# Kernel tuning notes

Hardware: AMD Instinct MI355X
Metric: run time of the kernel (lower is better)

The kernel has to match this reference:

```python
import math
import jax, jax.numpy as jnp
import numpy as np

RMS_EPS = 1.1920929e-07  # torch.finfo(float32).eps used by F.rms_norm default

def _rms_norm(x):
    return x * jax.lax.rsqrt(jnp.mean(jnp.square(x), axis=-1, keepdims=True) + RMS_EPS)

def _rope(x, cos, sin):
    # x: [B,T,H,D]; cos/sin: [T, D//2]
    d = x.shape[-1] // 2
    x1, x2 = x[..., :d], x[..., d:]
    c = cos[None, :, None, :]
    s = sin[None, :, None, :]
    return jnp.concatenate([x1 * c + x2 * s, -x1 * s + x2 * c], axis=-1).astype(x.dtype)

def setup_inputs():
    key = jax.random.key(0)
    ks = jax.random.split(key, 8)
    B, T, C, H, D = 2, 2048, 2048, 16, 128
    x = jax.random.normal(ks[0], (B, T, C), dtype=jnp.float32)
    # real RoPE tables for [T, D//2]
    half = D // 2
    inv_freq = 1.0 / (10000.0 ** (np.arange(half, dtype=np.float32) / half))
    ang = np.outer(np.arange(T, dtype=np.float32), inv_freq)
    cos = jnp.asarray(np.cos(ang), dtype=jnp.float32)
    sin = jnp.asarray(np.sin(ang), dtype=jnp.float32)
    s = 0.02
    Wq = jax.random.normal(ks[1], (C, H * D), dtype=jnp.float32) * s
    Wk = jax.random.normal(ks[2], (C, H * D), dtype=jnp.float32) * s
    Wv = jax.random.normal(ks[3], (C, H * D), dtype=jnp.float32) * s
    Wo = jax.random.normal(ks[4], (C, C), dtype=jnp.float32) * s
    fgate_w = jax.random.normal(ks[5], (C, H), dtype=jnp.float32) * s
    fgate_b = jnp.zeros((H,), dtype=jnp.float32)
    weight_lambda = jax.random.normal(ks[6], (C, H), dtype=jnp.float32) * s
    return dict(x=x, cos=cos, sin=sin, Wq=Wq, Wk=Wk, Wv=Wv, Wo=Wo,
                fgate_w=fgate_w, fgate_b=fgate_b, weight_lambda=weight_lambda,
                window_size=1024)

def reference(x, cos, sin, Wq, Wk, Wv, Wo, fgate_w, fgate_b, weight_lambda, window_size):
    B, T, C = x.shape
    H = fgate_w.shape[1]
    D = Wq.shape[1] // H
    sm_scale = 1.0 / math.sqrt(D)
    # QKV projections (bias=False)
    q = (x @ Wq).reshape(B, T, H, D)
    k = (x @ Wk).reshape(B, T, H, D)
    v = (x @ Wv).reshape(B, T, H, D)
    # RoPE then parameter-free RMSNorm on q,k
    q = _rms_norm(_rope(q, cos, sin))
    k = _rms_norm(_rope(k, cos, sin))
    # [B,H,T,D]
    q = q.transpose(0, 2, 1, 3)
    k = k.transpose(0, 2, 1, 3)
    v = v.transpose(0, 2, 1, 3)
    # forgetting gate: log f_t per (B,H,T)
    lam = jax.nn.elu((x @ weight_lambda).astype(jnp.float32)) + 1.0          # [B,T,H]
    logit = (x @ fgate_w + fgate_b) * lam                                    # [B,T,H]
    log_fgate = (jax.nn.log_sigmoid(logit) / (lam + 0.001)).transpose(0, 2, 1)  # [B,H,T]
    cumF = jnp.cumsum(log_fgate, axis=-1)                                    # [B,H,T]
    # forgetting flash attention, dense reference: bias_ij = cumF_i - cumF_j
    scores = jnp.einsum('bhqd,bhkd->bhqk', q.astype(jnp.float32), k.astype(jnp.float32)) * sm_scale
    scores = scores + cumF[..., :, None] - cumF[..., None, :]
    i = jnp.arange(T)[:, None]
    j = jnp.arange(T)[None, :]
    allowed = (j <= i) & (i - j < window_size)  # causal + sliding window
    scores = jnp.where(allowed, scores, -jnp.inf)
    attn = jax.nn.softmax(scores, axis=-1)
    y = jnp.einsum('bhqk,bhkd->bhqd', attn, v.astype(jnp.float32)).astype(x.dtype)
    y = y.transpose(0, 2, 1, 3).reshape(B, T, C)
    return y @ Wo
```

## Files before the change

### kernel.cpp

```cpp
#include <hip/hip_runtime.h>
#include <hip/hip_bf16.h>
#include <stdint.h>

#define T_SEQ 2048
#define CDIM  2048
#define NHEAD 16
#define DHEAD 128
#define BT    4096
#define BHT   32
#define NQKV  6144

typedef __bf16 bf16x8_t __attribute__((ext_vector_type(8)));
typedef float  f32x4_t  __attribute__((ext_vector_type(4)));
typedef unsigned short u16x8_t __attribute__((ext_vector_type(8)));
typedef unsigned short u16x4_t __attribute__((ext_vector_type(4)));

__device__ __forceinline__ unsigned short f2bf(float f){
  unsigned int u = __float_as_uint(f);
  u += 0x7fffu + ((u >> 16) & 1u);
  return (unsigned short)(u >> 16);
}
__device__ __forceinline__ float bf2f(unsigned short h){
  return __uint_as_float(((unsigned int)h) << 16);
}
__device__ __forceinline__ unsigned ldsaddr(const void* p){
  return (unsigned)(size_t)(const __attribute__((address_space(3))) void*)p;
}
__device__ __forceinline__ u16x4_t tr16(unsigned a){
  u16x4_t r;
  asm volatile("ds_read_b64_tr_b16 %0, %1" : "=v"(r) : "v"(a));
  return r;
}

__global__ __launch_bounds__(256) void transpose_cast(const float* __restrict__ W,
                                                      unsigned short* __restrict__ Wt){
  __shared__ float tile[32][33];
  int n0 = blockIdx.x*32, k0 = blockIdx.y*32;
  int tx = threadIdx.x, ty = threadIdx.y;
  #pragma unroll
  for (int i=0;i<32;i+=8)
    tile[ty+i][tx] = W[(size_t)(k0+ty+i)*CDIM + n0 + tx];
  __syncthreads();
  #pragma unroll
  for (int i=0;i<32;i+=8)
    Wt[(size_t)(n0+ty+i)*CDIM + k0 + tx] = f2bf(tile[tx][ty+i]);
}

__global__ __launch_bounds__(256) void build_wgt(const float* __restrict__ fgw,
                                                 const float* __restrict__ wlam,
                                                 float* __restrict__ WgT){
  int idx = blockIdx.x*256 + threadIdx.x;
  int c = idx >> 11, k = idx & 2047;
  const float* W = (c < 16) ? fgw : wlam;
  WgT[idx] = W[k*16 + (c & 15)];
}


#define V3_SYNC() do{ __builtin_amdgcn_sched_barrier(0); \
  __builtin_amdgcn_s_barrier(); \
  asm volatile("s_waitcnt lgkmcnt(0)" ::: "memory"); \
  __builtin_amdgcn_sched_barrier(0); }while(0)

#define V3_TAIL() do{ asm volatile("s_waitcnt vmcnt(3)" ::: "memory"); \
  __builtin_amdgcn_sched_barrier(0); \
  __builtin_amdgcn_s_barrier(); }while(0)

#define V3_MFMA() do{ __builtin_amdgcn_s_setprio(1); \
  _Pragma("unroll") for (int mi=0;mi<4;mi++) \
  _Pragma("unroll") for (int ni=0;ni<4;ni++) \
    acc[mi][ni] = __builtin_amdgcn_mfma_f32_16x16x32_bf16(af[mi], bfr[ni], acc[mi][ni],0,0,0); \
  __builtin_amdgcn_s_setprio(0); }while(0)

#define V3_PHASE(BUF, TIDX) do{ \
  readA(BUF); readB(BUF); \
  { int ts_ = (TIDX)+2; if (ts_ > ntm1) ts_ = ntm1; stage(((BUF)+2)%3, ts_); } \
  V3_SYNC(); V3_MFMA(); V3_TAIL(); }while(0)

template<int MODE>
__global__ __launch_bounds__(512, 2) void gemm_v3(const unsigned short* __restrict__ A,
                                                  const unsigned short* __restrict__ Bt,
                                                  void* __restrict__ Cout,
                                                  int M, int N, int K){
  extern __shared__ unsigned short lds[];
  const int nx = N >> 8;
  const int Mt = M >> 7;
  const int bid = blockIdx.x;
  const int c8 = bid & 7, w = bid >> 3;
  const int mh = Mt >> 1;
  const int mt = (c8 & 1)*mh + (w % mh);
  const int ntc = (c8 >> 1)*(nx >> 2) + (w / mh);
  const int m0 = mt << 7, n0 = ntc << 8;
  const int tid = threadIdx.x, lane = tid & 63, wv = tid >> 6;
  const int wm = wv >> 2, wn = wv & 3;
  const int g = lane >> 4, qi = lane & 15;
  const int ntm1 = (K >> 5) - 1;

  f32x4_t acc[4][4] = {};
  bf16x8_t af[4], bfr[4];

  int goffA, goffB[2];
  { int s = tid; int row = s >> 2; int lg = (s & 3) ^ ((row >> 1) & 3);
    goffA = row*K + lg*8; }
  #pragma unroll
  for (int j=0;j<2;j++){
    int s = j*512 + tid;
    int row = s >> 2;
    int lg = (s & 3) ^ ((row >> 1) & 3);
    goffB[j] = row*K + lg*8;
  }

  auto stage = [&](int buf, int kt){
    const unsigned short* srcA = A + (size_t)m0*K + kt*32;
    const unsigned short* srcB = Bt + (size_t)n0*K + kt*32;
    unsigned short* base = lds + buf*12288;
    __builtin_amdgcn_global_load_lds(
        (const __attribute__((address_space(1))) void*)(srcA + goffA),
        (__attribute__((address_space(3))) void*)(base + tid*8), 16, 0, 0);
    #pragma unroll
    for (int j=0;j<2;j++)
      __builtin_amdgcn_global_load_lds(
        (const __attribute__((address_space(1))) void*)(srcB + goffB[j]),
        (__attribute__((address_space(3))) void*)(base + 4096 + (j*512 + tid)*8), 16, 0, 0);
  };
  auto readA = [&](int buf){
    const unsigned short* base = lds + buf*12288;
    #pragma unroll
    for (int mi=0;mi<4;mi++){
      int row = wm*64 + mi*16 + qi;
      int gs = g ^ ((row >> 1) & 3);
      af[mi] = *reinterpret_cast<const bf16x8_t*>(base + (row*4 + gs)*8);
    }
  };
  auto readB = [&](int buf){
    const unsigned short* base = lds + buf*12288 + 4096;
    #pragma unroll
    for (int ni=0;ni<4;ni++){
      int row = wn*64 + ni*16 + qi;
      int gs = g ^ ((row >> 1) & 3);
      bfr[ni] = *reinterpret_cast<const bf16x8_t*>(base + (row*4 + gs)*8);
    }
  };

  stage(0,0); stage(1,1);
  asm volatile("s_waitcnt vmcnt(3)" ::: "memory");
  __builtin_amdgcn_sched_barrier(0);
  __builtin_amdgcn_s_barrier();

  for (int it=0; it<21; ++it){
    const int t3 = it*3;
    V3_PHASE(0, t3+0);
    V3_PHASE(1, t3+1);
    V3_PHASE(2, t3+2);
  }
  V3_PHASE(0, 63);
  asm volatile("s_waitcnt vmcnt(0)" ::: "memory");

  #pragma unroll
  for (int mi=0;mi<4;mi++){
    #pragma unroll
    for (int ni=0;ni<4;ni++){
      #pragma unroll
      for (int r=0;r<4;r++){
        int mm = m0 + wm*64 + mi*16 + 4*g + r;
        int nn = n0 + wn*64 + ni*16 + qi;
        float v = acc[mi][ni][r];
        if (MODE == 2){
          ((float*)Cout)[(size_t)mm*N + nn] = v;
        } else {
          int bb2 = mm >> 11, t = mm & (T_SEQ-1);
          int which = nn >> 11;
          int hh = (nn >> 7) & 15, d = nn & (DHEAD-1);
          ((unsigned short*)Cout)[(size_t)which*8388608 +
              (((size_t)bb2*NHEAD + hh)*T_SEQ + t)*DHEAD + d] = f2bf(v);
        }
      }
    }
  }
}

#define GROWS 4
__global__ __launch_bounds__(256) void gates_kernel(const float* __restrict__ x,
    const float* __restrict__ WgT, const float* __restrict__ fgb,
    float* __restrict__ lfg, unsigned short* __restrict__ xb){
  __shared__ float xs[GROWS*2048];
  __shared__ float part[GROWS*32*8];
  const int r0 = blockIdx.x*GROWS;
  const int tid = threadIdx.x;
  const float* xp = x + (size_t)r0*CDIM;
  #pragma unroll
  for (int i=0;i<GROWS*2048/(256*4); i++){
    int e = (i*256+tid)*4;
    *(float4*)(xs+e) = *(const float4*)(xp+e);
  }
  __syncthreads();
  #pragma unroll
  for (int i=0;i<GROWS*2048/(256*8); i++){
    int e = (i*256+tid)*8;
    u16x8_t ob;
    #pragma unroll
    for (int j=0;j<8;j++) ob[j] = f2bf(xs[e+j]);
    *reinterpret_cast<u16x8_t*>(xb + (size_t)r0*CDIM + e) = ob;
  }
  const int c = tid & 31, kseg = tid >> 5;
  const float* wp = WgT + c*2048 + kseg*256;
  const float* xq = xs + kseg*256;
  f32x4_t acc[GROWS] = {};
  for (int kk=0; kk<64; kk++){
    f32x4_t wv = *(const f32x4_t*)(wp + kk*4);
    #pragma unroll
    for (int r=0;r<GROWS;r++){
      f32x4_t xv = *(const f32x4_t*)(xq + r*2048 + kk*4);
      acc[r] += xv*wv;
    }
  }
  #pragma unroll
  for (int r=0;r<GROWS;r++)
    part[(r*32 + c)*8 + kseg] = acc[r][0]+acc[r][1]+acc[r][2]+acc[r][3];
  __syncthreads();
  if (tid < GROWS*32){
    const int r = tid >> 5, c2 = tid & 31;
    const float* pp = part + (r*32+c2)*8;
    float s = pp[0]+pp[1]+pp[2]+pp[3]+pp[4]+pp[5]+pp[6]+pp[7];
    float other = __shfl_xor(s, 16, 64);
    if (c2 < 16){
      float df = s, dl = other;
      float lam = (dl > 0.f) ? (dl + 1.f) : __expf(dl);
      float logit = (df + fgb[c2]) * lam;
      float ls = fminf(logit, 0.f) - log1pf(__expf(-fabsf(logit)));
      float lf = ls / (lam + 0.001f);
      int row = r0 + r;
      int b = row >> 11, t = row & (T_SEQ-1);
      lfg[((size_t)b*NHEAD + c2)*T_SEQ + t] = lf;
    }
  }
}

__global__ __launch_bounds__(256) void cumsum_kernel(const float* __restrict__ lfg,
                                                     float* __restrict__ cumF){
  __shared__ float sums[256];
  const int bh = blockIdx.x;
  const float* in = lfg + (size_t)bh*T_SEQ;
  float* out = cumF + (size_t)bh*T_SEQ;
  const int tid = threadIdx.x;
  float4 a = *(const float4*)(in + tid*8);
  float4 b = *(const float4*)(in + tid*8 + 4);
  float v[8] = {a.x,a.y,a.z,a.w,b.x,b.y,b.z,b.w};
  float run = 0.f;
  #pragma unroll
  for (int e=0;e<8;e++) run += v[e];
  sums[tid] = run;
  __syncthreads();
  for (int off=1; off<256; off<<=1){
    float y = (tid >= off) ? sums[tid-off] : 0.f;
    __syncthreads();
    sums[tid] += y;
    __syncthreads();
  }
  float acc = sums[tid] - run;
  float o[8];
  #pragma unroll
  for (int e=0;e<8;e++){ acc += v[e]; o[e] = acc; }
  *(float4*)(out + tid*8)     = make_float4(o[0],o[1],o[2],o[3]);
  *(float4*)(out + tid*8 + 4) = make_float4(o[4],o[5],o[6],o[7]);
}

__global__ __launch_bounds__(256) void rope_rms(unsigned short* __restrict__ QK,
    const float* __restrict__ cosT, const float* __restrict__ sinT){
  const int tid = threadIdx.x, lane = tid & 63, wv = tid >> 6;
  const int idx2 = blockIdx.x*4 + wv;
  const int which = idx2 >> 16;
  const int row = idx2 & 65535;
  const int t = row & (T_SEQ-1);
  unsigned short* xp = QK + (size_t)which*8388608 + (size_t)row*DHEAD;
  float x1 = bf2f(xp[lane]);
  float x2 = bf2f(xp[lane+64]);
  float c = cosT[t*64 + lane];
  float s = sinT[t*64 + lane];
  float o1 = x1*c + x2*s;
  float o2 = x2*c - x1*s;
  float ss = o1*o1 + o2*o2;
  #pragma unroll
  for (int off=1; off<64; off<<=1) ss += __shfl_xor(ss, off, 64);
  float scale = rsqrtf(ss*(1.f/128.f) + 1.1920929e-07f);
  xp[lane]    = f2bf(o1*scale);
  xp[lane+64] = f2bf(o2*scale);
}

__global__ __launch_bounds__(256, 2) void attn_kernel(const unsigned short* __restrict__ Qh,
    const unsigned short* __restrict__ Kh, const unsigned short* __restrict__ Vh,
    const float* __restrict__ cumF, unsigned short* __restrict__ Y,
    const int* __restrict__ winp){
  __shared__ unsigned short smem[32768];
  const int dlin = blockIdx.y*16 + blockIdx.x;
  const int c8 = dlin & 7, klin = dlin >> 3;
  const int bh = c8 + 8*(klin >> 4);
  const int q0b = (klin & 15)*128;
  const int b = bh >> 4, h = bh & 15;
  const int tid = threadIdx.x, lane = tid & 63, wv = tid >> 6;
  const int g = lane >> 4, qi = lane & 15;
  const int win = *winp;
  const unsigned short* Qp = Qh + (size_t)bh*T_SEQ*DHEAD;
  const unsigned short* Kp = Kh + (size_t)bh*T_SEQ*DHEAD;
  const unsigned short* Vp = Vh + (size_t)bh*T_SEQ*DHEAD;
  const float* cF = cumF + (size_t)bh*T_SEQ;
  const int q0w = q0b + wv*32;
  bf16x8_t qf[2][4];
  float cFq[2];
  #pragma unroll
  for (int qb=0;qb<2;qb++){
    cFq[qb] = cF[q0w + qb*16 + qi];
    #pragma unroll
    for (int dt=0;dt<4;dt++)
      qf[qb][dt] = *reinterpret_cast<const bf16x8_t*>(Qp + (size_t)(q0w + qb*16 + qi)*DHEAD + dt*32 + g*8);
  }
  f32x4_t ot[2][8] = {};
  float mrun[2] = {-1e30f, -1e30f}, lrun[2] = {0.f, 0.f};
  const float sm_scale = 0.08838834764831845f;
  int kbeg = q0b - win + 1; if (kbeg < 0) kbeg = 0; kbeg &= ~63;
  const int nt = (q0b + 128 - kbeg) >> 6;

  auto stage = [&](int bi, int k0s){
    unsigned short* Kd = smem + bi*8192;
    unsigned short* Vd = smem + 16384 + bi*8192;
    #pragma unroll
    for (int jj=0;jj<4;jj++){
      int t = (wv*4+jj)*64 + lane;
      int r = t>>4, cc = t&15;
      __builtin_amdgcn_global_load_lds(
        (const __attribute__((address_space(1))) void*)(Kp + (size_t)(k0s+r)*DHEAD + ((cc ^ (r&7))*8)),
        (__attribute__((address_space(3))) void*)(Kd + t*8), 16, 0, 0);
      int dd = t>>7, kq = (t>>3)&15, rr = (t>>1)&3, hb = t&1;
      __builtin_amdgcn_global_load_lds(
        (const __attribute__((address_space(1))) void*)(Vp + (size_t)(k0s + kq*4 + rr)*DHEAD + dd*16 + hb*8),
        (__attribute__((address_space(3))) void*)(Vd + t*8), 16, 0, 0);
    }
  };

  stage(0, kbeg);
  for (int it=0; it<nt; ++it){
    const int k0 = kbeg + it*64;
    const int cur = it & 1;
    __syncthreads();
    if (it+1 < nt) stage(cur^1, k0+64);
    if (k0 <= q0w+31 && (k0 + 63) >= (q0w - win + 1)){
      const unsigned short* Kc = smem + cur*8192;
      f32x4_t s[2][4] = {};
      __builtin_amdgcn_s_setprio(1);
      #pragma unroll
      for (int dt=0;dt<4;dt++){
        bf16x8_t kf[4];
        #pragma unroll
        for (int kb=0;kb<4;kb++){
          int row = kb*16 + qi;
          kf[kb] = *reinterpret_cast<const bf16x8_t*>(Kc + row*128 + (((dt*4+g) ^ (row&7))*8));
        }
        #pragma unroll
        for (int kb=0;kb<4;kb++){
          s[0][kb] = __builtin_amdgcn_mfma_f32_16x16x32_bf16(kf[kb], qf[0][dt], s[0][kb], 0,0,0);
          s[1][kb] = __builtin_amdgcn_mfma_f32_16x16x32_bf16(kf[kb], qf[1][dt], s[1][kb], 0,0,0);
        }
      }
      __builtin_amdgcn_s_setprio(0);
      float4 cb[4];
      #pragma unroll
      for (int kb=0;kb<4;kb++) cb[kb] = *(const float4*)(cF + k0 + kb*16 + 4*g);
      u16x8_t pb[2][2];
      #pragma unroll
      for (int qb=0;qb<2;qb++){
        const int qg = q0w + qb*16 + qi;
        float p[16], tmax = -INFINITY;
        #pragma unroll
        for (int kb=0;kb<4;kb++){
          #pragma unroll
          for (int r=0;r<4;r++){
            int key = k0 + kb*16 + 4*g + r;
            float sv = fmaf(s[qb][kb][r], sm_scale, cFq[qb] - ((const float*)&cb[kb])[r]);
            bool ok = (key <= qg) && (qg - key < win);
            p[kb*4+r] = ok ? sv : -INFINITY;
            tmax = fmaxf(tmax, p[kb*4+r]);
          }
        }
        tmax = fmaxf(tmax, __shfl_xor(tmax, 16, 64));
        tmax = fmaxf(tmax, __shfl_xor(tmax, 32, 64));
        float mnew = fmaxf(mrun[qb], tmax);
        float alpha = __expf(mrun[qb] - mnew);
        float tsum = 0.f;
        #pragma unroll
        for (int i2=0;i2<16;i2++){ p[i2] = __expf(p[i2] - mnew); tsum += p[i2]; }
        tsum += __shfl_xor(tsum, 16, 64);
        tsum += __shfl_xor(tsum, 32, 64);
        lrun[qb] = lrun[qb]*alpha + tsum;
        mrun[qb] = mnew;
        #pragma unroll
        for (int dt=0;dt<8;dt++) ot[qb][dt] *= alpha;
        #pragma unroll
        for (int cc=0;cc<2;cc++){
          #pragma unroll
          for (int e=0;e<8;e++)
            pb[qb][cc][e] = f2bf(p[(2*cc + (e>>2))*4 + (e&3)]);
        }
      }
      unsigned vbase = ldsaddr(smem + 16384 + cur*8192) + lane*8;
      #pragma unroll
      for (int cc=0;cc<2;cc++){
        u16x4_t vlo[8], vhi[8];
        #pragma unroll
        for (int dt=0;dt<8;dt++){
          vlo[dt] = tr16(vbase + (unsigned)((dt*16 + 8*cc)*128));
          vhi[dt] = tr16(vbase + (unsigned)((dt*16 + 8*cc + 4)*128));
        }
        asm volatile("s_waitcnt lgkmcnt(0)");
        __builtin_amdgcn_sched_barrier(0);
        __builtin_amdgcn_s_setprio(1);
        #pragma unroll
        for (int dt=0;dt<8;dt++){
          u16x8_t vv = __builtin_shufflevector(vlo[dt], vhi[dt], 0,1,2,3,4,5,6,7);
          bf16x8_t vf = *reinterpret_cast<bf16x8_t*>(&vv);
          ot[0][dt] = __builtin_amdgcn_mfma_f32_16x16x32_bf16(vf, *reinterpret_cast<bf16x8_t*>(&pb[0][cc]), ot[0][dt], 0,0,0);
          ot[1][dt] = __builtin_amdgcn_mfma_f32_16x16x32_bf16(vf, *reinterpret_cast<bf16x8_t*>(&pb[1][cc]), ot[1][dt], 0,0,0);
        }
        __builtin_amdgcn_s_setprio(0);
      }
    }
  }
  __syncthreads();
  float invl[2] = {1.f/lrun[0], 1.f/lrun[1]};
  #pragma unroll
  for (int qb=0;qb<2;qb++){
    int qlocal = wv*32 + qb*16 + qi;
    #pragma unroll
    for (int dt=0;dt<8;dt++){
      int d8 = dt*2 + (g>>1);
      u16x4_t w;
      #pragma unroll
      for (int r=0;r<4;r++) w[r] = f2bf(ot[qb][dt][r]*invl[qb]);
      *reinterpret_cast<u16x4_t*>(smem + qlocal*128 + ((d8 ^ (qlocal&7))*8) + 4*(g&1)) = w;
    }
  }
  __syncthreads();
  #pragma unroll
  for (int i=0;i<8;i++){
    int t = i*256 + tid;
    int row = t>>4, cc = t&15;
    u16x8_t v = *reinterpret_cast<const u16x8_t*>(smem + row*128 + ((cc ^ (row&7))*8));
    *reinterpret_cast<u16x8_t*>(Y + ((size_t)b*T_SEQ + q0b + row)*CDIM + h*DHEAD + cc*8) = v;
  }
}

extern "C" void kernel_launch(void* const* d_in, const int* in_sizes, int n_in,
                              void* d_out, int out_size, void* d_ws, size_t ws_size,
                              hipStream_t stream){
  const float* x    = (const float*)d_in[0];
  const float* cosT = (const float*)d_in[1];
  const float* sinT = (const float*)d_in[2];
  const float* Wq   = (const float*)d_in[3];
  const float* Wk   = (const float*)d_in[4];
  const float* Wv   = (const float*)d_in[5];
  const float* Wo   = (const float*)d_in[6];
  const float* fgw  = (const float*)d_in[7];
  const float* fgb  = (const float*)d_in[8];
  const float* wlam = (const float*)d_in[9];
  const int*   winp = (const int*)d_in[10];

  char* ws = (char*)d_ws;
  unsigned short* xb    = (unsigned short*)(ws + 0);
  unsigned short* WqkvT = (unsigned short*)(ws + 16777216);
  unsigned short* WoT   = (unsigned short*)(ws + 41943040);
  unsigned short* QKVh  = (unsigned short*)(ws + 50331648);
  unsigned short* Qh = QKVh;
  unsigned short* Kh = QKVh + 8388608;
  unsigned short* Vh = QKVh + 16777216;
  unsigned short* Yb  = (unsigned short*)(ws + 100663296);
  float* lfg  = (float*)(ws + 117440512);
  float* cumF = (float*)(ws + 117702656);
  float* WgT  = (float*)(ws + 117964800);

  build_wgt<<<256, 256, 0, stream>>>(fgw, wlam, WgT);
  gates_kernel<<<BT/GROWS, 256, 0, stream>>>(x, WgT, fgb, lfg, xb);
  cumsum_kernel<<<BHT, 256, 0, stream>>>(lfg, cumF);

  dim3 tgrid(64,64), tblk(32,8);
  transpose_cast<<<tgrid, tblk, 0, stream>>>(Wq, WqkvT);
  transpose_cast<<<tgrid, tblk, 0, stream>>>(Wk, WqkvT + 4194304);
  transpose_cast<<<tgrid, tblk, 0, stream>>>(Wv, WqkvT + 8388608);
  transpose_cast<<<tgrid, tblk, 0, stream>>>(Wo, WoT);

  hipFuncSetAttribute(reinterpret_cast<const void*>(&gemm_v3<1>),
      hipFuncAttributeMaxDynamicSharedMemorySize, 73728);
  hipFuncSetAttribute(reinterpret_cast<const void*>(&gemm_v3<2>),
      hipFuncAttributeMaxDynamicSharedMemorySize, 73728);

  gemm_v3<1><<<(BT/128)*(NQKV/256), 512, 73728, stream>>>(xb, WqkvT, QKVh, BT, NQKV, CDIM);

  rope_rms<<<2*BHT*T_SEQ/4, 256, 0, stream>>>(QKVh, cosT, sinT);

  attn_kernel<<<dim3(16, BHT), 256, 0, stream>>>(Qh, Kh, Vh, cumF, Yb, winp);

  gemm_v3<2><<<(BT/128)*(CDIM/256), 512, 73728, stream>>>(Yb, WoT, d_out, BT, CDIM, CDIM);
}
```

Before: 290.2 us.

## Fuse RoPE and RMSNorm into QKV GEMM epilogue; merge weight transposes

The QKV GEMM epilogue now stages Q/K tiles in LDS as bf16, then applies RoPE and RMS normalisation per head row before writing to the head-major layout. This removes the separate rope_rms kernel and its read-modify-write pass over Q and K. The four weight transpose launches are also merged into one launch with a z dimension. In exchange the epilogue adds an LDS round trip, an extra barrier and serial per-row work per wave, and it rounds to bf16 twice before normalisation.

```diff
diff --git a/kernel.cpp b/kernel.cpp
--- a/kernel.cpp
+++ b/kernel.cpp
@@ -32,9 +32,14 @@
   return r;
 }
 
-__global__ __launch_bounds__(256) void transpose_cast(const float* __restrict__ W,
-                                                      unsigned short* __restrict__ Wt){
+__global__ __launch_bounds__(256) void transpose_all(const float* __restrict__ Wq,
+    const float* __restrict__ Wk, const float* __restrict__ Wv,
+    const float* __restrict__ Wo, unsigned short* __restrict__ WqkvT,
+    unsigned short* __restrict__ WoT){
   __shared__ float tile[32][33];
+  const int z = blockIdx.z;
+  const float* W = (z==0)?Wq:(z==1)?Wk:(z==2)?Wv:Wo;
+  unsigned short* Wt = (z<3) ? (WqkvT + (size_t)z*4194304) : WoT;
   int n0 = blockIdx.x*32, k0 = blockIdx.y*32;
   int tx = threadIdx.x, ty = threadIdx.y;
   #pragma unroll
@@ -55,7 +60,6 @@
   WgT[idx] = W[k*16 + (c & 15)];
 }
 
-
 #define V3_SYNC() do{ __builtin_amdgcn_sched_barrier(0); \
   __builtin_amdgcn_s_barrier(); \
   asm volatile("s_waitcnt lgkmcnt(0)" ::: "memory"); \
@@ -80,6 +84,8 @@
 __global__ __launch_bounds__(512, 2) void gemm_v3(const unsigned short* __restrict__ A,
                                                   const unsigned short* __restrict__ Bt,
                                                   void* __restrict__ Cout,
+                                                  const float* __restrict__ cosT,
+                                                  const float* __restrict__ sinT,
                                                   int M, int N, int K){
   extern __shared__ unsigned short lds[];
   const int nx = N >> 8;
@@ -155,25 +161,73 @@
   V3_PHASE(0, 63);
   asm volatile("s_waitcnt vmcnt(0)" ::: "memory");
 
-  #pragma unroll
-  for (int mi=0;mi<4;mi++){
-    #pragma unroll
-    for (int ni=0;ni<4;ni++){
-      #pragma unroll
-      for (int r=0;r<4;r++){
-        int mm = m0 + wm*64 + mi*16 + 4*g + r;
-        int nn = n0 + wn*64 + ni*16 + qi;
-        float v = acc[mi][ni][r];
-        if (MODE == 2){
-          ((float*)Cout)[(size_t)mm*N + nn] = v;
-        } else {
+  if (MODE == 2){
+    #pragma unroll
+    for (int mi=0;mi<4;mi++)
+      #pragma unroll
+      for (int ni=0;ni<4;ni++)
+        #pragma unroll
+        for (int r=0;r<4;r++){
+          int mm = m0 + wm*64 + mi*16 + 4*g + r;
+          int nn = n0 + wn*64 + ni*16 + qi;
+          ((float*)Cout)[(size_t)mm*N + nn] = acc[mi][ni][r];
+        }
+    return;
+  }
+  const int which = n0 >> 11;
+  if (which == 2){
+    #pragma unroll
+    for (int mi=0;mi<4;mi++)
+      #pragma unroll
+      for (int ni=0;ni<4;ni++)
+        #pragma unroll
+        for (int r=0;r<4;r++){
+          int mm = m0 + wm*64 + mi*16 + 4*g + r;
+          int nn = n0 + wn*64 + ni*16 + qi;
           int bb2 = mm >> 11, t = mm & (T_SEQ-1);
-          int which = nn >> 11;
           int hh = (nn >> 7) & 15, d = nn & (DHEAD-1);
-          ((unsigned short*)Cout)[(size_t)which*8388608 +
-              (((size_t)bb2*NHEAD + hh)*T_SEQ + t)*DHEAD + d] = f2bf(v);
+          ((unsigned short*)Cout)[(size_t)2*8388608 +
+              (((size_t)bb2*NHEAD + hh)*T_SEQ + t)*DHEAD + d] = f2bf(acc[mi][ni][r]);
+        }
+    return;
+  }
+  __builtin_amdgcn_s_barrier();
+  {
+    unsigned short* X = lds;
+    #pragma unroll
+    for (int mi=0;mi<4;mi++){
+      #pragma unroll
+      for (int ni=0;ni<4;ni++){
+        int col = wn*64 + ni*16 + qi;
+        int d = col & 127, hl = col >> 7;
+        #pragma unroll
+        for (int r=0;r<4;r++){
+          int tl = wm*64 + mi*16 + 4*g + r;
+          X[(hl*128 + tl)*128 + d] = f2bf(acc[mi][ni][r]);
         }
       }
+    }
+    __syncthreads();
+    unsigned short* dst = (unsigned short*)Cout + (size_t)which*8388608;
+    const int h0 = (n0 & 2047) >> 7;
+    for (int j=0;j<32;j++){
+      int rho = wv*32 + j;
+      int hl = rho >> 7, tl = rho & 127;
+      int mm = m0 + tl;
+      int b = mm >> 11, t = mm & (T_SEQ-1);
+      float x1 = bf2f(X[rho*128 + lane]);
+      float x2 = bf2f(X[rho*128 + lane + 64]);
+      float c = cosT[t*64 + lane];
+      float s = sinT[t*64 + lane];
+      float o1 = x1*c + x2*s;
+      float o2 = x2*c - x1*s;
+      float ssum = o1*o1 + o2*o2;
+      #pragma unroll
+      for (int off=1; off<64; off<<=1) ssum += __shfl_xor(ssum, off, 64);
+      float scale = rsqrtf(ssum*(1.f/128.f) + 1.1920929e-07f);
+      unsigned short* rowp = dst + (((size_t)b*NHEAD + h0 + hl)*T_SEQ + t)*DHEAD;
+      rowp[lane]      = f2bf(o1*scale);
+      rowp[lane + 64] = f2bf(o2*scale);
     }
   }
 }
@@ -262,28 +316,6 @@
   for (int e=0;e<8;e++){ acc += v[e]; o[e] = acc; }
   *(float4*)(out + tid*8)     = make_float4(o[0],o[1],o[2],o[3]);
   *(float4*)(out + tid*8 + 4) = make_float4(o[4],o[5],o[6],o[7]);
-}
-
-__global__ __launch_bounds__(256) void rope_rms(unsigned short* __restrict__ QK,
-    const float* __restrict__ cosT, const float* __restrict__ sinT){
-  const int tid = threadIdx.x, lane = tid & 63, wv = tid >> 6;
-  const int idx2 = blockIdx.x*4 + wv;
-  const int which = idx2 >> 16;
-  const int row = idx2 & 65535;
-  const int t = row & (T_SEQ-1);
-  unsigned short* xp = QK + (size_t)which*8388608 + (size_t)row*DHEAD;
-  float x1 = bf2f(xp[lane]);
-  float x2 = bf2f(xp[lane+64]);
-  float c = cosT[t*64 + lane];
-  float s = sinT[t*64 + lane];
-  float o1 = x1*c + x2*s;
-  float o2 = x2*c - x1*s;
-  float ss = o1*o1 + o2*o2;
-  #pragma unroll
-  for (int off=1; off<64; off<<=1) ss += __shfl_xor(ss, off, 64);
-  float scale = rsqrtf(ss*(1.f/128.f) + 1.1920929e-07f);
-  xp[lane]    = f2bf(o1*scale);
-  xp[lane+64] = f2bf(o2*scale);
 }
 
 __global__ __launch_bounds__(256, 2) void attn_kernel(const unsigned short* __restrict__ Qh,
@@ -479,22 +511,16 @@
   gates_kernel<<<BT/GROWS, 256, 0, stream>>>(x, WgT, fgb, lfg, xb);
   cumsum_kernel<<<BHT, 256, 0, stream>>>(lfg, cumF);
 
-  dim3 tgrid(64,64), tblk(32,8);
-  transpose_cast<<<tgrid, tblk, 0, stream>>>(Wq, WqkvT);
-  transpose_cast<<<tgrid, tblk, 0, stream>>>(Wk, WqkvT + 4194304);
-  transpose_cast<<<tgrid, tblk, 0, stream>>>(Wv, WqkvT + 8388608);
-  transpose_cast<<<tgrid, tblk, 0, stream>>>(Wo, WoT);
+  transpose_all<<<dim3(64,64,4), dim3(32,8), 0, stream>>>(Wq, Wk, Wv, Wo, WqkvT, WoT);
 
   hipFuncSetAttribute(reinterpret_cast<const void*>(&gemm_v3<1>),
       hipFuncAttributeMaxDynamicSharedMemorySize, 73728);
   hipFuncSetAttribute(reinterpret_cast<const void*>(&gemm_v3<2>),
       hipFuncAttributeMaxDynamicSharedMemorySize, 73728);
 
-  gemm_v3<1><<<(BT/128)*(NQKV/256), 512, 73728, stream>>>(xb, WqkvT, QKVh, BT, NQKV, CDIM);
-
-  rope_rms<<<2*BHT*T_SEQ/4, 256, 0, stream>>>(QKVh, cosT, sinT);
+  gemm_v3<1><<<(BT/128)*(NQKV/256), 512, 73728, stream>>>(xb, WqkvT, QKVh, cosT, sinT, BT, NQKV, CDIM);
 
   attn_kernel<<<dim3(16, BHT), 256, 0, stream>>>(Qh, Kh, Vh, cumF, Yb, winp);
 
-  gemm_v3<2><<<(BT/128)*(CDIM/256), 512, 73728, stream>>>(Yb, WoT, d_out, BT, CDIM, CDIM);
-}
+  gemm_v3<2><<<(BT/128)*(CDIM/256), 512, 73728, stream>>>(Yb, WoT, d_out, nullptr, nullptr, BT, CDIM, CDIM);
+}
```

Result: slower. 316.5 us (+9.1%).
